# Kernel optimization log

Measured on AMD Instinct MI355X. Metric: run time of the kernel, lower is better.

Reference implementation:

```python
import jax, jax.numpy as jnp
import numpy as np

B, S, D, H = 4, 2048, 768, 12
HD = D // H
SCALE = HD ** -0.5


def setup_inputs() -> dict:
    key = jax.random.key(0)
    ks = jax.random.split(key, 9)
    std = D ** -0.5
    x = jax.random.normal(ks[0], (B, S, D), dtype=jnp.float32)
    Wq = jax.random.normal(ks[1], (D, D), dtype=jnp.float32) * std
    Wk = jax.random.normal(ks[2], (D, D), dtype=jnp.float32) * std
    Wv = jax.random.normal(ks[3], (D, D), dtype=jnp.float32) * std
    Wo = jax.random.normal(ks[4], (D, D), dtype=jnp.float32) * std
    bq = jax.random.normal(ks[5], (D,), dtype=jnp.float32) * 0.01
    bk = jax.random.normal(ks[6], (D,), dtype=jnp.float32) * 0.01
    bv = jax.random.normal(ks[7], (D,), dtype=jnp.float32) * 0.01
    bo = jax.random.normal(ks[8], (D,), dtype=jnp.float32) * 0.01
    return {"x": x, "Wq": Wq, "bq": bq, "Wk": Wk, "bk": bk,
            "Wv": Wv, "bv": bv, "Wo": Wo, "bo": bo}


def reference(x, Wq, bq, Wk, bk, Wv, bv, Wo, bo):
    b, s, _ = x.shape
    # projections (torch Linear: y = x @ W.T + b)
    q = (x @ Wq.T + bq).reshape(b, s, H, HD).transpose(0, 2, 1, 3)  # [B,H,S,HD]
    k = (x @ Wk.T + bk).reshape(b, s, H, HD).transpose(0, 2, 1, 3)
    v = (x @ Wv.T + bv).reshape(b, s, H, HD).transpose(0, 2, 1, 3)
    attn = jnp.einsum('bhqd,bhkd->bhqk', q, k) * SCALE
    attn = jax.nn.softmax(attn, axis=-1)  # dropout is identity in eval mode
    out = jnp.einsum('bhqk,bhkd->bhqd', attn, v)
    out = out.transpose(0, 2, 1, 3).reshape(b, s, D)
    return out @ Wo.T + bo
```

## Files before the change

kernel.cpp:

```cpp
#include <hip/hip_runtime.h>

#define LOG2E 1.4426950408889634f
#define QSCALE (0.125f * LOG2E)

typedef __attribute__((ext_vector_type(8))) __bf16 bf8_t;
typedef __attribute__((ext_vector_type(4))) float f4_t;

__device__ __forceinline__ unsigned short f2bf(float f) {
  unsigned int u = __float_as_uint(f);
  u += 0x7fff + ((u >> 16) & 1);
  return (unsigned short)(u >> 16);
}

__device__ __forceinline__ void async16(const void* g, void* l) {
  __builtin_amdgcn_global_load_lds(
      (const __attribute__((address_space(1))) void*)g,
      (__attribute__((address_space(3))) void*)l, 16, 0, 0);
}

__device__ __forceinline__ int swm(int r) {
  return ((r & 3) << 4) | ((r & 8) << 3);
}
__device__ __forceinline__ int swzoff(int row, int cb) {
  return (row << 7) + (cb ^ swm(row));
}

__global__ void cvt_multi(const float* __restrict__ x,
                          const float* __restrict__ w0, const float* __restrict__ w1,
                          const float* __restrict__ w2, const float* __restrict__ w3,
                          unsigned short* __restrict__ xb,
                          unsigned short* __restrict__ d0, unsigned short* __restrict__ d1,
                          unsigned short* __restrict__ d2, unsigned short* __restrict__ d3) {
  const int NX = 1572864;
  const int NW = 147456;
  const int total = NX + 4 * NW;
  int i = blockIdx.x * blockDim.x + threadIdx.x;
  int stride = gridDim.x * blockDim.x;
  for (; i < total; i += stride) {
    const float* s;
    unsigned short* d;
    int off;
    if (i < NX) {
      s = x; d = xb; off = i;
    } else {
      int j = i - NX;
      int wsel = j / NW;
      off = j - wsel * NW;
      s = (wsel == 0) ? w0 : (wsel == 1) ? w1 : (wsel == 2) ? w2 : w3;
      d = (wsel == 0) ? d0 : (wsel == 1) ? d1 : (wsel == 2) ? d2 : d3;
    }
    float4 v = ((const float4*)s)[off];
    ushort4 o;
    o.x = f2bf(v.x); o.y = f2bf(v.y); o.z = f2bf(v.z); o.w = f2bf(v.w);
    ((ushort4*)d)[off] = o;
  }
}

__device__ __forceinline__ void gemm_core64(const unsigned short* __restrict__ A,
                                            const unsigned short* __restrict__ Bm,
                                            int i0, int j0, char* ls,
                                            f4_t (&acc)[4][2]) {
  const int tid = threadIdx.x, l = tid & 63;
  const int wi = (tid >> 6) >> 1, wj = (tid >> 6) & 1;
  auto stage = [&](int buf, int k0) {
    char* dA = ls + buf * 24576;
    char* dB = dA + 16384;
#pragma unroll
    for (int u = 0; u < 4; ++u) {
      int p = (u * 256 + tid) * 16;
      int r = p >> 7, c = (p & 127) ^ swm(r);
      async16((const char*)A + ((size_t)(i0 + r) * 768 + k0) * 2 + c, dA + p);
    }
#pragma unroll
    for (int u = 0; u < 2; ++u) {
      int p = (u * 256 + tid) * 16;
      int r = p >> 7, c = (p & 127) ^ swm(r);
      async16((const char*)Bm + ((size_t)(j0 + r) * 768 + k0) * 2 + c, dB + p);
    }
  };
  stage(0, 0);
  for (int kk = 0; kk < 12; ++kk) {
    if (kk < 11) {
      stage((kk + 1) & 1, (kk + 1) * 64);
      asm volatile("s_waitcnt vmcnt(6)" ::: "memory");
    } else {
      asm volatile("s_waitcnt vmcnt(0)" ::: "memory");
    }
    __builtin_amdgcn_s_barrier();
    const char* lsA = ls + (kk & 1) * 24576;
    const char* lsB = lsA + 16384;
#pragma unroll
    for (int ks = 0; ks < 2; ++ks) {
      bf8_t af[4], bfr[2];
#pragma unroll
      for (int mi = 0; mi < 4; ++mi)
        af[mi] = *(const bf8_t*)(lsA + swzoff(wi * 64 + mi * 16 + (l & 15),
                                              ks * 64 + ((l >> 4) << 4)));
#pragma unroll
      for (int nj = 0; nj < 2; ++nj)
        bfr[nj] = *(const bf8_t*)(lsB + swzoff(wj * 32 + nj * 16 + (l & 15),
                                               ks * 64 + ((l >> 4) << 4)));
      __builtin_amdgcn_s_setprio(1);
#pragma unroll
      for (int mi = 0; mi < 4; ++mi)
#pragma unroll
        for (int nj = 0; nj < 2; ++nj)
          acc[mi][nj] = __builtin_amdgcn_mfma_f32_16x16x32_bf16(
              af[mi], bfr[nj], acc[mi][nj], 0, 0, 0);
      __builtin_amdgcn_s_setprio(0);
    }
    __builtin_amdgcn_s_barrier();
  }
}

__global__ __launch_bounds__(256) void proj_qkv(
    const unsigned short* __restrict__ xb,
    const unsigned short* __restrict__ wq,
    const unsigned short* __restrict__ wk,
    const unsigned short* __restrict__ wv,
    const float* __restrict__ bq, const float* __restrict__ bk,
    const float* __restrict__ bv,
    unsigned short* __restrict__ qo, unsigned short* __restrict__ ko,
    unsigned short* __restrict__ vto) {
  __shared__ char ls[49152];
  const int bx = (blockIdx.x & 7) * 288 + (blockIdx.x >> 3);
  const int mt = bx / 18, nt = bx % 18;
  const int sec = nt / 6, nn = nt % 6;
  f4_t acc[4][2] = {};
  int i0, j0;
  if (sec < 2) {
    i0 = nn * 128;
    j0 = mt * 64;
    gemm_core64(sec ? wk : wq, xb, i0, j0, ls, acc);
  } else {
    i0 = (mt >> 1) * 128;
    j0 = (nn * 2 + (mt & 1)) * 64;
    gemm_core64(xb, wv, i0, j0, ls, acc);
  }

  const int tid = threadIdx.x, l = tid & 63;
  const int wi = (tid >> 6) >> 1, wj = (tid >> 6) & 1;
#pragma unroll
  for (int mi = 0; mi < 4; ++mi) {
#pragma unroll
    for (int nj = 0; nj < 2; ++nj) {
      int ib = wi * 64 + mi * 16 + ((l >> 4) << 2);
      int j  = wj * 32 + nj * 16 + (l & 15);
      f4_t v = acc[mi][nj];
      ushort4 o;
      if (sec < 2) {
        const float* bias = sec ? bk : bq;
        float sc = sec ? 1.0f : QSCALE;
        float4 bs = *(const float4*)(bias + i0 + ib);
        o.x = f2bf((v[0] + bs.x) * sc);
        o.y = f2bf((v[1] + bs.y) * sc);
        o.z = f2bf((v[2] + bs.z) * sc);
        o.w = f2bf((v[3] + bs.w) * sc);
      } else {
        float bvs = bv[j0 + j];
        o.x = f2bf(v[0] + bvs); o.y = f2bf(v[1] + bvs);
        o.z = f2bf(v[2] + bvs); o.w = f2bf(v[3] + bvs);
      }
      int chunk = (ib >> 3) ^ (j & 15);
      *(ushort4*)(ls + j * 256 + chunk * 16 + ((ib & 7) << 1)) = o;
    }
  }
  __syncthreads();
  const int row = tid >> 2, q4 = tid & 3;
  if (sec < 2) {
    int sg = mt * 64 + row;
    int b = sg >> 11, s = sg & 2047;
    unsigned short* base = sec ? ko : qo;
#pragma unroll
    for (int cc = 0; cc < 4; ++cc) {
      int cb = q4 * 4 + cc;
      uint4 v = *(const uint4*)(ls + row * 256 + ((cb ^ (row & 15)) << 4));
      int h = nn * 2 + (cb >> 3);
      *(uint4*)(base + (((size_t)(b * 12 + h) * 2048 + s) << 6) + (cb & 7) * 8) = v;
    }
  } else {
    int h = nn * 2 + (mt & 1), dh = row;
    int st = mt >> 1;
    int b = st >> 4;
    int sl = (st & 15) * 128;
    unsigned short* dst0 = vto + ((size_t)((b * 12 + h) * 64 + dh)) * 2048 + sl;
#pragma unroll
    for (int cc = 0; cc < 4; ++cc) {
      int cb = q4 * 4 + cc;
      uint4 v = *(const uint4*)(ls + row * 256 + ((cb ^ (row & 15)) << 4));
      *(uint4*)(dst0 + cb * 8) = v;
    }
  }
}

__global__ __launch_bounds__(256) void proj_o(
    const unsigned short* __restrict__ attnb, const unsigned short* __restrict__ wo,
    const float* __restrict__ bo, float* __restrict__ outp) {
  __shared__ char ls[49152];
  const int bx = (blockIdx.x & 7) * 96 + (blockIdx.x >> 3);
  const int it = bx % 6, jt = bx / 6;
  const int i0 = it * 128, j0 = jt * 64;
  f4_t acc[4][2] = {};
  gemm_core64(wo, attnb, i0, j0, ls, acc);
  const int tid = threadIdx.x, l = tid & 63;
  const int wi = (tid >> 6) >> 1, wj = (tid >> 6) & 1;
#pragma unroll
  for (int mi = 0; mi < 4; ++mi) {
#pragma unroll
    for (int nj = 0; nj < 2; ++nj) {
      int ib = i0 + wi * 64 + mi * 16 + ((l >> 4) << 2);
      int j  = j0 + wj * 32 + nj * 16 + (l & 15);
      float4 bs = *(const float4*)(bo + ib);
      float4 o;
      o.x = acc[mi][nj][0] + bs.x;
      o.y = acc[mi][nj][1] + bs.y;
      o.z = acc[mi][nj][2] + bs.z;
      o.w = acc[mi][nj][3] + bs.w;
      *(float4*)(outp + (size_t)j * 768 + ib) = o;
    }
  }
}

__global__ __launch_bounds__(512) void attn_kernel(
    const unsigned short* __restrict__ qg,
    const unsigned short* __restrict__ kg,
    const unsigned short* __restrict__ vtg,
    unsigned short* __restrict__ attnb) {
  __shared__ char ls[65536];
  const int tid = threadIdx.x, l = tid & 63, w = tid >> 6;
  const int qw = w & 3, hf = w >> 2;
  const int swz = (blockIdx.x & 7) * 96 + (blockIdx.x >> 3);
  const int q0 = (swz & 15) * 128;
  const int bh = swz >> 4;
  const size_t qkbase = (size_t)bh * 2048 * 64;
  const size_t vtbase = (size_t)bh * 64 * 2048;

#pragma unroll
  for (int u = 0; u < 2; ++u) {
    int p = (u * 512 + tid) * 16;
    int r = p >> 7, cb = p & 127;
    int c = cb ^ swm(r);
    async16((const char*)qg + (qkbase + (size_t)(q0 + r) * 64) * 2 + c, ls + p);
  }
  __syncthreads();
  bf8_t qf[2][2];
#pragma unroll
  for (int qt = 0; qt < 2; ++qt)
#pragma unroll
    for (int ks = 0; ks < 2; ++ks)
      qf[qt][ks] = *(const bf8_t*)(ls + swzoff(qw * 32 + qt * 16 + (l & 15),
                                               ks * 64 + ((l >> 4) << 4)));
  __syncthreads();

  const int p16 = tid * 16;
  const int sr = p16 >> 7;
  const int sc = (p16 & 127) ^ swm(sr);
  async16((const char*)kg + (qkbase + (size_t)sr * 64) * 2 + sc, ls + p16);
  async16((const char*)vtg + (vtbase + (size_t)sr * 2048) * 2 + sc,
          ls + 8192 + p16);
  async16((const char*)kg + (qkbase + (size_t)(64 + sr) * 64) * 2 + sc,
          ls + 16384 + p16);
  async16((const char*)vtg + (vtbase + (size_t)sr * 2048 + 64) * 2 + sc,
          ls + 16384 + 8192 + p16);
  const char* gKa = (const char*)kg + (qkbase + (size_t)(128 + sr) * 64) * 2 + sc;
  const char* gVa = (const char*)vtg + (vtbase + (size_t)sr * 2048 + 128) * 2 + sc;
  const char* gKb = gKa + 8192;
  const char* gVb = gVa + 128;
  __syncthreads();

  int koff[4][2];
#pragma unroll
  for (int kt = 0; kt < 4; ++kt) {
    int i = l & 15;
    int row = ((kt >> 1) << 5) + ((kt & 1) << 2) + ((i >> 2) << 3) + (i & 3);
#pragma unroll
    for (int ks = 0; ks < 2; ++ks)
      koff[kt][ks] = swzoff(row, ks * 64 + ((l >> 4) << 4));
  }
  int voff[4][2];
#pragma unroll
  for (int dt = 0; dt < 4; ++dt)
#pragma unroll
    for (int ks = 0; ks < 2; ++ks)
      voff[dt][ks] = swzoff(dt * 16 + (l & 15), ks * 64 + ((l >> 4) << 4));

  bf8_t onesf;
#pragma unroll
  for (int e = 0; e < 8; ++e) onesf[e] = (__bf16)1.0f;

  f4_t acc[4][2] = {};
  f4_t accs[2] = {};

  for (int i = 0; i < 16; ++i) {
    if (i < 15) {
      char* dst = ls + (((i + 1) & 1) * 2) * 16384;
      async16(gKa, dst + p16);
      async16(gVa, dst + 8192 + p16);
      async16(gKb, dst + 16384 + p16);
      async16(gVb, dst + 16384 + 8192 + p16);
      gKa += 16384; gKb += 16384;
      gVa += 256;   gVb += 256;
    }
    const char* bK = ls + ((i & 1) * 2 + hf) * 16384;
    const char* bV = bK + 8192;

    f4_t sacc[4][2] = {};
    __builtin_amdgcn_s_setprio(1);
#pragma unroll
    for (int kt = 0; kt < 4; ++kt)
#pragma unroll
      for (int ks = 0; ks < 2; ++ks) {
        bf8_t a = *(const bf8_t*)(bK + koff[kt][ks]);
#pragma unroll
        for (int qt = 0; qt < 2; ++qt)
          sacc[kt][qt] = __builtin_amdgcn_mfma_f32_16x16x32_bf16(
              a, qf[qt][ks], sacc[kt][qt], 0, 0, 0);
      }
    __builtin_amdgcn_s_setprio(0);

    bf8_t pf[2][2];
#pragma unroll
    for (int qt = 0; qt < 2; ++qt)
#pragma unroll
      for (int ks = 0; ks < 2; ++ks)
#pragma unroll
        for (int e = 0; e < 8; ++e)
          pf[ks][qt][e] =
              (__bf16)__builtin_amdgcn_exp2f(sacc[2 * ks + (e >> 2)][qt][e & 3]);

    __builtin_amdgcn_s_setprio(1);
#pragma unroll
    for (int dt = 0; dt < 4; ++dt) {
      bf8_t av0 = *(const bf8_t*)(bV + voff[dt][0]);
      bf8_t av1 = *(const bf8_t*)(bV + voff[dt][1]);
#pragma unroll
      for (int qt = 0; qt < 2; ++qt) {
        acc[dt][qt] = __builtin_amdgcn_mfma_f32_16x16x32_bf16(av0, pf[0][qt],
                                                              acc[dt][qt], 0, 0, 0);
        acc[dt][qt] = __builtin_amdgcn_mfma_f32_16x16x32_bf16(av1, pf[1][qt],
                                                              acc[dt][qt], 0, 0, 0);
      }
    }
#pragma unroll
    for (int qt = 0; qt < 2; ++qt) {
      accs[qt] = __builtin_amdgcn_mfma_f32_16x16x32_bf16(onesf, pf[0][qt],
                                                         accs[qt], 0, 0, 0);
      accs[qt] = __builtin_amdgcn_mfma_f32_16x16x32_bf16(onesf, pf[1][qt],
                                                         accs[qt], 0, 0, 0);
    }
    __builtin_amdgcn_s_setprio(0);
    __syncthreads();
  }

  char* reg_ = ls + qw * 8704;
  if (hf) {
#pragma unroll
    for (int dt = 0; dt < 4; ++dt)
#pragma unroll
      for (int qt = 0; qt < 2; ++qt)
        *(f4_t*)(reg_ + (((dt * 2 + qt) * 64) + l) * 16) = acc[dt][qt];
    *(float2*)(reg_ + 8192 + l * 8) = float2{accs[0][0], accs[1][0]};
  }
  __syncthreads();
  if (!hf) {
    const int bb = bh / 12, h = bh % 12;
    float2 os = *(const float2*)(reg_ + 8192 + l * 8);
    float inv0 = 1.0f / (accs[0][0] + os.x);
    float inv1 = 1.0f / (accs[1][0] + os.y);
#pragma unroll
    for (int qt = 0; qt < 2; ++qt) {
      float inv = qt ? inv1 : inv0;
      int s = q0 + qw * 32 + qt * 16 + (l & 15);
#pragma unroll
      for (int dt = 0; dt < 4; ++dt) {
        f4_t other = *(const f4_t*)(reg_ + (((dt * 2 + qt) * 64) + l) * 16);
        int dg = h * 64 + dt * 16 + ((l >> 4) << 2);
        ushort4 o;
        o.x = f2bf((acc[dt][qt][0] + other[0]) * inv);
        o.y = f2bf((acc[dt][qt][1] + other[1]) * inv);
        o.z = f2bf((acc[dt][qt][2] + other[2]) * inv);
        o.w = f2bf((acc[dt][qt][3] + other[3]) * inv);
        *(ushort4*)(attnb + ((size_t)(bb * 2048 + s)) * 768 + dg) = o;
      }
    }
  }
}

extern "C" void kernel_launch(void* const* d_in, const int* in_sizes, int n_in,
                              void* d_out, int out_size, void* d_ws, size_t ws_size,
                              hipStream_t stream) {
  const float* x  = (const float*)d_in[0];
  const float* Wq = (const float*)d_in[1];
  const float* bq = (const float*)d_in[2];
  const float* Wk = (const float*)d_in[3];
  const float* bk = (const float*)d_in[4];
  const float* Wv = (const float*)d_in[5];
  const float* bv = (const float*)d_in[6];
  const float* Wo = (const float*)d_in[7];
  const float* bo = (const float*)d_in[8];

  const size_t XB_ELEMS = (size_t)8192 * 768;
  const size_t W_ELEMS  = (size_t)768 * 768;
  unsigned short* xb  = (unsigned short*)d_ws;
  unsigned short* wqb = xb  + XB_ELEMS;
  unsigned short* wkb = wqb + W_ELEMS;
  unsigned short* wvb = wkb + W_ELEMS;
  unsigned short* wob = wvb + W_ELEMS;
  unsigned short* qb  = wob + W_ELEMS;
  unsigned short* kb  = qb  + XB_ELEMS;
  unsigned short* vtb = kb  + XB_ELEMS;
  unsigned short* attnb = xb;

  cvt_multi<<<2048, 256, 0, stream>>>(x, Wq, Wk, Wv, Wo,
                                      xb, wqb, wkb, wvb, wob);
  proj_qkv<<<2304, 256, 0, stream>>>(xb, wqb, wkb, wvb, bq, bk, bv, qb, kb, vtb);
  attn_kernel<<<768, 512, 0, stream>>>(qb, kb, vtb, attnb);
  proj_o<<<768, 256, 0, stream>>>(attnb, wob, bo, (float*)d_out);
}
```

Baseline: 130.1 us.

## Fuse x fp32-to-bf16 conversion into QKV projection and unify V tile path

The separate pass that converted x to bf16 is removed. The QKV projection now reads fp32 x directly, converts it in registers and writes it to swizzled LDS, while the weight tiles keep using async global-to-LDS loads. The V section now uses the same tile mapping as Q and K and transposes through LDS with a padded layout when storing V^T. This removes a full write and re-read of bf16 x, but each block now reads x as fp32 (twice the bytes) and does the conversion on the critical path, and the load/compute overlap changes from async loads to register prefetch.

Result: slower. 138.9 us (+6.8%).

```diff
diff --git a/kernel.cpp b/kernel.cpp
--- a/kernel.cpp
+++ b/kernel.cpp
@@ -25,96 +25,26 @@
   return (row << 7) + (cb ^ swm(row));
 }
 
-__global__ void cvt_multi(const float* __restrict__ x,
-                          const float* __restrict__ w0, const float* __restrict__ w1,
-                          const float* __restrict__ w2, const float* __restrict__ w3,
-                          unsigned short* __restrict__ xb,
-                          unsigned short* __restrict__ d0, unsigned short* __restrict__ d1,
-                          unsigned short* __restrict__ d2, unsigned short* __restrict__ d3) {
-  const int NX = 1572864;
-  const int NW = 147456;
-  const int total = NX + 4 * NW;
+__global__ void cvt4_kernel(const float* __restrict__ s0, const float* __restrict__ s1,
+                            const float* __restrict__ s2, const float* __restrict__ s3,
+                            unsigned short* __restrict__ d0, unsigned short* __restrict__ d1,
+                            unsigned short* __restrict__ d2, unsigned short* __restrict__ d3,
+                            int n4) {
+  int z = blockIdx.y;
+  const float* s = (z == 0) ? s0 : (z == 1) ? s1 : (z == 2) ? s2 : s3;
+  unsigned short* d = (z == 0) ? d0 : (z == 1) ? d1 : (z == 2) ? d2 : d3;
   int i = blockIdx.x * blockDim.x + threadIdx.x;
   int stride = gridDim.x * blockDim.x;
-  for (; i < total; i += stride) {
-    const float* s;
-    unsigned short* d;
-    int off;
-    if (i < NX) {
-      s = x; d = xb; off = i;
-    } else {
-      int j = i - NX;
-      int wsel = j / NW;
-      off = j - wsel * NW;
-      s = (wsel == 0) ? w0 : (wsel == 1) ? w1 : (wsel == 2) ? w2 : w3;
-      d = (wsel == 0) ? d0 : (wsel == 1) ? d1 : (wsel == 2) ? d2 : d3;
-    }
-    float4 v = ((const float4*)s)[off];
+  for (; i < n4; i += stride) {
+    float4 v = ((const float4*)s)[i];
     ushort4 o;
     o.x = f2bf(v.x); o.y = f2bf(v.y); o.z = f2bf(v.z); o.w = f2bf(v.w);
-    ((ushort4*)d)[off] = o;
-  }
-}
-
-__device__ __forceinline__ void gemm_core64(const unsigned short* __restrict__ A,
-                                            const unsigned short* __restrict__ Bm,
-                                            int i0, int j0, char* ls,
-                                            f4_t (&acc)[4][2]) {
-  const int tid = threadIdx.x, l = tid & 63;
-  const int wi = (tid >> 6) >> 1, wj = (tid >> 6) & 1;
-  auto stage = [&](int buf, int k0) {
-    char* dA = ls + buf * 24576;
-    char* dB = dA + 16384;
-#pragma unroll
-    for (int u = 0; u < 4; ++u) {
-      int p = (u * 256 + tid) * 16;
-      int r = p >> 7, c = (p & 127) ^ swm(r);
-      async16((const char*)A + ((size_t)(i0 + r) * 768 + k0) * 2 + c, dA + p);
-    }
-#pragma unroll
-    for (int u = 0; u < 2; ++u) {
-      int p = (u * 256 + tid) * 16;
-      int r = p >> 7, c = (p & 127) ^ swm(r);
-      async16((const char*)Bm + ((size_t)(j0 + r) * 768 + k0) * 2 + c, dB + p);
-    }
-  };
-  stage(0, 0);
-  for (int kk = 0; kk < 12; ++kk) {
-    if (kk < 11) {
-      stage((kk + 1) & 1, (kk + 1) * 64);
-      asm volatile("s_waitcnt vmcnt(6)" ::: "memory");
-    } else {
-      asm volatile("s_waitcnt vmcnt(0)" ::: "memory");
-    }
-    __builtin_amdgcn_s_barrier();
-    const char* lsA = ls + (kk & 1) * 24576;
-    const char* lsB = lsA + 16384;
-#pragma unroll
-    for (int ks = 0; ks < 2; ++ks) {
-      bf8_t af[4], bfr[2];
-#pragma unroll
-      for (int mi = 0; mi < 4; ++mi)
-        af[mi] = *(const bf8_t*)(lsA + swzoff(wi * 64 + mi * 16 + (l & 15),
-                                              ks * 64 + ((l >> 4) << 4)));
-#pragma unroll
-      for (int nj = 0; nj < 2; ++nj)
-        bfr[nj] = *(const bf8_t*)(lsB + swzoff(wj * 32 + nj * 16 + (l & 15),
-                                               ks * 64 + ((l >> 4) << 4)));
-      __builtin_amdgcn_s_setprio(1);
-#pragma unroll
-      for (int mi = 0; mi < 4; ++mi)
-#pragma unroll
-        for (int nj = 0; nj < 2; ++nj)
-          acc[mi][nj] = __builtin_amdgcn_mfma_f32_16x16x32_bf16(
-              af[mi], bfr[nj], acc[mi][nj], 0, 0, 0);
-      __builtin_amdgcn_s_setprio(0);
-    }
-    __builtin_amdgcn_s_barrier();
+    ((ushort4*)d)[i] = o;
   }
 }
 
 __global__ __launch_bounds__(256) void proj_qkv(
-    const unsigned short* __restrict__ xb,
+    const float* __restrict__ xf,
     const unsigned short* __restrict__ wq,
     const unsigned short* __restrict__ wk,
     const unsigned short* __restrict__ wv,
@@ -126,48 +56,102 @@
   const int bx = (blockIdx.x & 7) * 288 + (blockIdx.x >> 3);
   const int mt = bx / 18, nt = bx % 18;
   const int sec = nt / 6, nn = nt % 6;
-  f4_t acc[4][2] = {};
-  int i0, j0;
-  if (sec < 2) {
-    i0 = nn * 128;
-    j0 = mt * 64;
-    gemm_core64(sec ? wk : wq, xb, i0, j0, ls, acc);
-  } else {
-    i0 = (mt >> 1) * 128;
-    j0 = (nn * 2 + (mt & 1)) * 64;
-    gemm_core64(xb, wv, i0, j0, ls, acc);
-  }
+  const int i0 = nn * 128;
+  const int j0 = mt * 64;
+  const unsigned short* A = (sec == 0) ? wq : (sec == 1) ? wk : wv;
 
   const int tid = threadIdx.x, l = tid & 63;
   const int wi = (tid >> 6) >> 1, wj = (tid >> 6) & 1;
-#pragma unroll
-  for (int mi = 0; mi < 4; ++mi) {
-#pragma unroll
-    for (int nj = 0; nj < 2; ++nj) {
-      int ib = wi * 64 + mi * 16 + ((l >> 4) << 2);
-      int j  = wj * 32 + nj * 16 + (l & 15);
-      f4_t v = acc[mi][nj];
-      ushort4 o;
-      if (sec < 2) {
+
+  const int xrow = tid >> 2;
+  const int xcb = (tid & 3) * 32;
+  const float* xbase = xf + (size_t)(j0 + xrow) * 768 + (xcb >> 1);
+  float4 xr0, xr1, xr2, xr3;
+  auto xload = [&](int k0) {
+    const float4* g = (const float4*)(xbase + k0);
+    xr0 = g[0]; xr1 = g[1]; xr2 = g[2]; xr3 = g[3];
+  };
+  auto pk2 = [](float lo, float hi) -> unsigned {
+    return (unsigned)f2bf(lo) | ((unsigned)f2bf(hi) << 16);
+  };
+  auto xwrite = [&](int buf) {
+    char* dB = ls + buf * 24576 + 16384 + (xrow << 7);
+    uint4 w0{pk2(xr0.x, xr0.y), pk2(xr0.z, xr0.w),
+             pk2(xr1.x, xr1.y), pk2(xr1.z, xr1.w)};
+    uint4 w1{pk2(xr2.x, xr2.y), pk2(xr2.z, xr2.w),
+             pk2(xr3.x, xr3.y), pk2(xr3.z, xr3.w)};
+    *(uint4*)(dB + (xcb ^ swm(xrow))) = w0;
+    *(uint4*)(dB + ((xcb + 16) ^ swm(xrow))) = w1;
+  };
+  auto wstage = [&](int buf, int k0) {
+    char* dA = ls + buf * 24576;
+#pragma unroll
+    for (int u = 0; u < 4; ++u) {
+      int p = (u * 256 + tid) * 16;
+      int r = p >> 7, c = (p & 127) ^ swm(r);
+      async16((const char*)A + ((size_t)(i0 + r) * 768 + k0) * 2 + c, dA + p);
+    }
+  };
+
+  f4_t acc[4][2] = {};
+  xload(0);
+  wstage(0, 0);
+  xwrite(0);
+  __syncthreads();
+  for (int kk = 0; kk < 12; ++kk) {
+    const int buf = kk & 1;
+    if (kk < 11) {
+      xload((kk + 1) * 64);
+      wstage(buf ^ 1, (kk + 1) * 64);
+    }
+    const char* lsA = ls + buf * 24576;
+    const char* lsB = lsA + 16384;
+#pragma unroll
+    for (int ks = 0; ks < 2; ++ks) {
+      bf8_t af[4], bfr[2];
+#pragma unroll
+      for (int mi = 0; mi < 4; ++mi)
+        af[mi] = *(const bf8_t*)(lsA + swzoff(wi * 64 + mi * 16 + (l & 15),
+                                              ks * 64 + ((l >> 4) << 4)));
+#pragma unroll
+      for (int nj = 0; nj < 2; ++nj)
+        bfr[nj] = *(const bf8_t*)(lsB + swzoff(wj * 32 + nj * 16 + (l & 15),
+                                               ks * 64 + ((l >> 4) << 4)));
+      __builtin_amdgcn_s_setprio(1);
+#pragma unroll
+      for (int mi = 0; mi < 4; ++mi)
+#pragma unroll
+        for (int nj = 0; nj < 2; ++nj)
+          acc[mi][nj] = __builtin_amdgcn_mfma_f32_16x16x32_bf16(
+              af[mi], bfr[nj], acc[mi][nj], 0, 0, 0);
+      __builtin_amdgcn_s_setprio(0);
+    }
+    if (kk < 11) xwrite(buf ^ 1);
+    __syncthreads();
+  }
+
+  if (sec < 2) {
+#pragma unroll
+    for (int mi = 0; mi < 4; ++mi) {
+#pragma unroll
+      for (int nj = 0; nj < 2; ++nj) {
+        int ib = wi * 64 + mi * 16 + ((l >> 4) << 2);
+        int j  = wj * 32 + nj * 16 + (l & 15);
+        f4_t v = acc[mi][nj];
         const float* bias = sec ? bk : bq;
         float sc = sec ? 1.0f : QSCALE;
         float4 bs = *(const float4*)(bias + i0 + ib);
+        ushort4 o;
         o.x = f2bf((v[0] + bs.x) * sc);
         o.y = f2bf((v[1] + bs.y) * sc);
         o.z = f2bf((v[2] + bs.z) * sc);
         o.w = f2bf((v[3] + bs.w) * sc);
-      } else {
-        float bvs = bv[j0 + j];
-        o.x = f2bf(v[0] + bvs); o.y = f2bf(v[1] + bvs);
-        o.z = f2bf(v[2] + bvs); o.w = f2bf(v[3] + bvs);
+        int chunk = (ib >> 3) ^ (j & 15);
+        *(ushort4*)(ls + j * 256 + chunk * 16 + ((ib & 7) << 1)) = o;
       }
-      int chunk = (ib >> 3) ^ (j & 15);
-      *(ushort4*)(ls + j * 256 + chunk * 16 + ((ib & 7) << 1)) = o;
-    }
-  }
-  __syncthreads();
-  const int row = tid >> 2, q4 = tid & 3;
-  if (sec < 2) {
+    }
+    __syncthreads();
+    const int row = tid >> 2, q4 = tid & 3;
     int sg = mt * 64 + row;
     int b = sg >> 11, s = sg & 2047;
     unsigned short* base = sec ? ko : qo;
@@ -179,17 +163,88 @@
       *(uint4*)(base + (((size_t)(b * 12 + h) * 2048 + s) << 6) + (cb & 7) * 8) = v;
     }
   } else {
-    int h = nn * 2 + (mt & 1), dh = row;
-    int st = mt >> 1;
-    int b = st >> 4;
-    int sl = (st & 15) * 128;
-    unsigned short* dst0 = vto + ((size_t)((b * 12 + h) * 64 + dh)) * 2048 + sl;
-#pragma unroll
-    for (int cc = 0; cc < 4; ++cc) {
-      int cb = q4 * 4 + cc;
-      uint4 v = *(const uint4*)(ls + row * 256 + ((cb ^ (row & 15)) << 4));
-      *(uint4*)(dst0 + cb * 8) = v;
-    }
+#pragma unroll
+    for (int mi = 0; mi < 4; ++mi) {
+#pragma unroll
+      for (int nj = 0; nj < 2; ++nj) {
+        int ib = wi * 64 + mi * 16 + ((l >> 4) << 2);
+        int j  = wj * 32 + nj * 16 + (l & 15);
+        f4_t v = acc[mi][nj];
+        float4 bs = *(const float4*)(bv + i0 + ib);
+#pragma unroll
+        for (int e = 0; e < 4; ++e) {
+          float b4 = (e == 0) ? bs.x : (e == 1) ? bs.y : (e == 2) ? bs.z : bs.w;
+          *(unsigned short*)(ls + (ib + e) * 144 + j * 2) = f2bf(v[e] + b4);
+        }
+      }
+    }
+    __syncthreads();
+    const int d = tid >> 1, half = tid & 1;
+    int h = nn * 2 + (d >> 6), dh = d & 63;
+    int b = mt >> 5;
+    int sl = (mt & 31) * 64 + half * 32;
+    unsigned short* dst = vto + ((size_t)((b * 12 + h) * 64 + dh)) * 2048 + sl;
+    const char* src = ls + d * 144 + half * 64;
+#pragma unroll
+    for (int c = 0; c < 4; ++c)
+      *(uint4*)(dst + c * 8) = *(const uint4*)(src + c * 16);
+  }
+}
+
+__device__ __forceinline__ void gemm_core64(const unsigned short* __restrict__ A,
+                                            const unsigned short* __restrict__ Bm,
+                                            int i0, int j0, char* ls,
+                                            f4_t (&acc)[4][2]) {
+  const int tid = threadIdx.x, l = tid & 63;
+  const int wi = (tid >> 6) >> 1, wj = (tid >> 6) & 1;
+  auto stage = [&](int buf, int k0) {
+    char* dA = ls + buf * 24576;
+    char* dB = dA + 16384;
+#pragma unroll
+    for (int u = 0; u < 4; ++u) {
+      int p = (u * 256 + tid) * 16;
+      int r = p >> 7, c = (p & 127) ^ swm(r);
+      async16((const char*)A + ((size_t)(i0 + r) * 768 + k0) * 2 + c, dA + p);
+    }
+#pragma unroll
+    for (int u = 0; u < 2; ++u) {
+      int p = (u * 256 + tid) * 16;
+      int r = p >> 7, c = (p & 127) ^ swm(r);
+      async16((const char*)Bm + ((size_t)(j0 + r) * 768 + k0) * 2 + c, dB + p);
+    }
+  };
+  stage(0, 0);
+  for (int kk = 0; kk < 12; ++kk) {
+    if (kk < 11) {
+      stage((kk + 1) & 1, (kk + 1) * 64);
+      asm volatile("s_waitcnt vmcnt(6)" ::: "memory");
+    } else {
+      asm volatile("s_waitcnt vmcnt(0)" ::: "memory");
+    }
+    __builtin_amdgcn_s_barrier();
+    const char* lsA = ls + (kk & 1) * 24576;
+    const char* lsB = lsA + 16384;
+#pragma unroll
+    for (int ks = 0; ks < 2; ++ks) {
+      bf8_t af[4], bfr[2];
+#pragma unroll
+      for (int mi = 0; mi < 4; ++mi)
+        af[mi] = *(const bf8_t*)(lsA + swzoff(wi * 64 + mi * 16 + (l & 15),
+                                              ks * 64 + ((l >> 4) << 4)));
+#pragma unroll
+      for (int nj = 0; nj < 2; ++nj)
+        bfr[nj] = *(const bf8_t*)(lsB + swzoff(wj * 32 + nj * 16 + (l & 15),
+                                               ks * 64 + ((l >> 4) << 4)));
+      __builtin_amdgcn_s_setprio(1);
+#pragma unroll
+      for (int mi = 0; mi < 4; ++mi)
+#pragma unroll
+        for (int nj = 0; nj < 2; ++nj)
+          acc[mi][nj] = __builtin_amdgcn_mfma_f32_16x16x32_bf16(
+              af[mi], bfr[nj], acc[mi][nj], 0, 0, 0);
+      __builtin_amdgcn_s_setprio(0);
+    }
+    __builtin_amdgcn_s_barrier();
   }
 }
 
@@ -401,19 +456,19 @@
 
   const size_t XB_ELEMS = (size_t)8192 * 768;
   const size_t W_ELEMS  = (size_t)768 * 768;
-  unsigned short* xb  = (unsigned short*)d_ws;
-  unsigned short* wqb = xb  + XB_ELEMS;
+  unsigned short* wqb = (unsigned short*)d_ws;
   unsigned short* wkb = wqb + W_ELEMS;
   unsigned short* wvb = wkb + W_ELEMS;
   unsigned short* wob = wvb + W_ELEMS;
   unsigned short* qb  = wob + W_ELEMS;
   unsigned short* kb  = qb  + XB_ELEMS;
   unsigned short* vtb = kb  + XB_ELEMS;
-  unsigned short* attnb = xb;
-
-  cvt_multi<<<2048, 256, 0, stream>>>(x, Wq, Wk, Wv, Wo,
-                                      xb, wqb, wkb, wvb, wob);
-  proj_qkv<<<2304, 256, 0, stream>>>(xb, wqb, wkb, wvb, bq, bk, bv, qb, kb, vtb);
+  unsigned short* attnb = vtb + XB_ELEMS;
+
+  cvt4_kernel<<<dim3(144, 4), 256, 0, stream>>>(Wq, Wk, Wv, Wo,
+                                                wqb, wkb, wvb, wob,
+                                                (int)(W_ELEMS / 4));
+  proj_qkv<<<2304, 256, 0, stream>>>(x, wqb, wkb, wvb, bq, bk, bv, qb, kb, vtb);
   attn_kernel<<<768, 512, 0, stream>>>(qb, kb, vtb, attnb);
   proj_o<<<768, 256, 0, stream>>>(attnb, wob, bo, (float*)d_out);
 }
```
